# Optimization experiments

Hardware: AMD Instinct MI355X
Metric: run time of the kernel (lower is better)

Reference implementation:

```python
import jax, jax.numpy as jnp
import numpy as np

MARGIN = 0.3  # hard-coded in all three MarginRankingLoss instances


def setup_inputs() -> dict:
    key = jax.random.key(0)
    k1, k2, k3, k4 = jax.random.split(key, 4)
    n, d, num_ids = 4096, 2048, 100
    inputs = jax.random.normal(k1, (n, d), dtype=jnp.float32)
    targets_a = jax.random.randint(k2, (n,), 0, num_ids, dtype=jnp.int64)
    targets_b = jax.random.randint(k3, (n,), 0, num_ids, dtype=jnp.int64)
    lam = jax.random.uniform(k4, (), dtype=jnp.float32)
    epoch = 60
    return {"inputs": inputs, "targets_a": targets_a, "targets_b": targets_b,
            "lam": lam, "epoch": epoch}


def reference(inputs, targets_a, targets_b, lam, epoch):
    # pairwise euclidean distance: dist[i,j] = ||x_i - x_j||
    sq = jnp.sum(inputs * inputs, axis=1)                      # [n]
    dist = sq[:, None] + sq[None, :] - 2.0 * (inputs @ inputs.T)
    dist = jnp.sqrt(jnp.clip(dist, 1e-12))                     # [n, n]

    ma = targets_a[:, None] == targets_a[None, :]
    mb = targets_b[:, None] == targets_b[None, :]
    m_same_ab = ma & mb                                        # same a AND b (incl. diagonal)
    m_same_or = (ma & ~mb) | (~ma & mb)                        # exactly one of a/b matches
    m_dif_ab = ~ma & ~mb                                       # neither matches

    ninf = -jnp.inf
    pinf = jnp.inf
    hp = jnp.max(jnp.where(m_same_ab, dist, ninf), axis=1)     # hardest positive
    hn = jnp.min(jnp.where(m_dif_ab, dist, pinf), axis=1)      # hardest negative
    max_or = jnp.max(jnp.where(m_same_or, dist, ninf), axis=1)
    min_or = jnp.min(jnp.where(m_same_or, dist, pinf), axis=1)

    use_or = m_same_or.any(axis=1) & (epoch > 50)
    sp = jnp.where(use_or, max_or, hp)
    sn = jnp.where(use_or, min_or, hn)

    # MarginRankingLoss(x1, x2, y=1) = mean(relu(x2 - x1 + margin))
    loss_1 = jnp.mean(jnp.maximum(0.0, hp - hn + MARGIN))
    loss_2 = jnp.mean(jnp.maximum(0.0, sp - hn + MARGIN))
    loss_3 = jnp.mean(jnp.maximum(0.0, hp - sn + MARGIN))
    return loss_1 + loss_2 + loss_3
```

## Files before the change

### kernel.cpp

```cpp
#include <hip/hip_runtime.h>
#include <hip/hip_bf16.h>

#define NROW 4096
#define KDIM 2048
#define ROWB (KDIM * 2)
#define BT 256
#define BK 32
#define NT (KDIM / BK)
#define LDSBUF 32768
#define PHI(r) ((((r) >> 1) & 3) << 4)

typedef __attribute__((ext_vector_type(8))) short bf16x8;
typedef __attribute__((ext_vector_type(4))) float f32x4;
typedef __attribute__((ext_vector_type(4))) unsigned short u16x4;

__device__ __forceinline__ unsigned short f2bf(float x) {
    unsigned u = __float_as_uint(x);
    unsigned r = (u + 0x7FFFu + ((u >> 16) & 1u)) >> 16;
    return (unsigned short)r;
}
__device__ __forceinline__ float bf2f(unsigned short b) {
    return __uint_as_float(((unsigned)b) << 16);
}

__global__ __launch_bounds__(256) void k_convert(const float* __restrict__ X,
                                                 unsigned short* __restrict__ Xb,
                                                 float* __restrict__ sqv) {
    const int row = blockIdx.x;
    const int t = threadIdx.x;
    const float4* xr = (const float4*)(X + (size_t)row * KDIM);
    unsigned short* br = Xb + (size_t)row * KDIM;
    float acc = 0.f;
#pragma unroll
    for (int it = 0; it < 2; ++it) {
        int idx = t * 2 + it;
        float4 v = xr[idx];
        u16x4 b;
        b.x = f2bf(v.x); b.y = f2bf(v.y); b.z = f2bf(v.z); b.w = f2bf(v.w);
        float f0 = bf2f(b.x), f1 = bf2f(b.y), f2 = bf2f(b.z), f3 = bf2f(b.w);
        acc += f0 * f0 + f1 * f1 + f2 * f2 + f3 * f3;
        *(u16x4*)(br + idx * 4) = b;
    }
#pragma unroll
    for (int s = 32; s > 0; s >>= 1) acc += __shfl_xor(acc, s);
    __shared__ float red[4];
    const int lane = t & 63, wid = t >> 6;
    if (lane == 0) red[wid] = acc;
    __syncthreads();
    if (t == 0) sqv[row] = red[0] + red[1] + red[2] + red[3];
}

__global__ __launch_bounds__(256) void k_init(unsigned* hp, unsigned* hn,
                                              unsigned* mor, unsigned* mir,
                                              int* anyor, float* out) {
    int i = blockIdx.x * 256 + threadIdx.x;
    hp[i] = 0u;
    hn[i] = 0x7F800000u;
    mor[i] = 0u;
    mir[i] = 0x7F800000u;
    anyor[i] = 0;
    if (i == 0) out[0] = 0.f;
}

__global__ __launch_bounds__(512, 2) void k_gemm(const unsigned short* __restrict__ Xb,
                                                 const float* __restrict__ sqv,
                                                 const int* __restrict__ ta,
                                                 const int* __restrict__ tb,
                                                 unsigned int* __restrict__ hp,
                                                 unsigned int* __restrict__ hn,
                                                 unsigned int* __restrict__ mor,
                                                 unsigned int* __restrict__ mir,
                                                 int* __restrict__ anyor) {
    __shared__ char lds[3 * LDSBUF];
    const int bi = blockIdx.x >> 4;
    const int bj = blockIdx.x & 15;
    const int t = threadIdx.x;
    const int lane = t & 63;
    const int w = t >> 6;
    const int wm = w >> 2;
    const int wn = w & 3;
    const int l15 = lane & 15;
    const int k16 = (lane >> 4) * 16;

    const int srow = w * 16 + (lane >> 2);
    const int scol = (lane & 3) * 16;
    const char* xbase = (const char*)Xb;

    int aoffs[8], boffs[4];
#pragma unroll
    for (int m = 0; m < 8; ++m) {
        int r = wm * 128 + m * 16 + l15;
        aoffs[m] = r * 64 + (k16 ^ PHI(r));
    }
#pragma unroll
    for (int n = 0; n < 4; ++n) {
        int j = wn * 64 + n * 16 + l15;
        boffs[n] = 16384 + j * 64 + (k16 ^ PHI(j));
    }

    f32x4 acc[8][4] = {};

#define STAGE(tt, p)                                                          \
    do {                                                                      \
        const int isb_ = (p) >> 1, half_ = (p) & 1;                           \
        const int R_ = half_ * 128 + srow;                                    \
        const int gr_ = (isb_ ? bj : bi) * BT + R_;                           \
        const char* gsrc_ = xbase + (size_t)gr_ * ROWB + (size_t)(tt) * 64 +  \
                            (scol ^ PHI(R_));                                 \
        char* ldst_ = lds + ((tt) % 3) * LDSBUF + isb_ * 16384 + R_ * 64 + scol; \
        __builtin_amdgcn_global_load_lds(                                     \
            (const __attribute__((address_space(1))) void*)gsrc_,             \
            (__attribute__((address_space(3))) void*)ldst_, 16, 0, 0);        \
    } while (0)

#pragma unroll
    for (int p = 0; p < 4; ++p) STAGE(0, p);
#pragma unroll
    for (int p = 0; p < 4; ++p) STAGE(1, p);

    bf16x8 af[4], bfr[4];
    for (int tk = 0; tk < NT; ++tk) {
        if (tk < NT - 1)
            asm volatile("s_waitcnt vmcnt(4)" ::: "memory");
        else
            asm volatile("s_waitcnt vmcnt(0)" ::: "memory");
        __builtin_amdgcn_s_barrier();
        __builtin_amdgcn_sched_barrier(0);
        const char* Ab = lds + (tk % 3) * LDSBUF;
        const bool st = (tk + 2) < NT;
        const int t2 = tk + 2;

        if (st) STAGE(t2, 0);
#pragma unroll
        for (int m = 0; m < 4; ++m) af[m] = *(const bf16x8*)(Ab + aoffs[m]);
        bfr[0] = *(const bf16x8*)(Ab + boffs[0]);
        bfr[1] = *(const bf16x8*)(Ab + boffs[1]);
        __builtin_amdgcn_s_barrier();
        __builtin_amdgcn_s_setprio(1);
#pragma unroll
        for (int m = 0; m < 4; ++m) {
            acc[m][0] = __builtin_amdgcn_mfma_f32_16x16x32_bf16(af[m], bfr[0], acc[m][0], 0, 0, 0);
            acc[m][1] = __builtin_amdgcn_mfma_f32_16x16x32_bf16(af[m], bfr[1], acc[m][1], 0, 0, 0);
        }
        __builtin_amdgcn_s_setprio(0);
        __builtin_amdgcn_s_barrier();

        if (st) STAGE(t2, 1);
        bfr[2] = *(const bf16x8*)(Ab + boffs[2]);
        bfr[3] = *(const bf16x8*)(Ab + boffs[3]);
        __builtin_amdgcn_s_barrier();
        __builtin_amdgcn_s_setprio(1);
#pragma unroll
        for (int m = 0; m < 4; ++m) {
            acc[m][2] = __builtin_amdgcn_mfma_f32_16x16x32_bf16(af[m], bfr[2], acc[m][2], 0, 0, 0);
            acc[m][3] = __builtin_amdgcn_mfma_f32_16x16x32_bf16(af[m], bfr[3], acc[m][3], 0, 0, 0);
        }
        __builtin_amdgcn_s_setprio(0);
        __builtin_amdgcn_s_barrier();

        if (st) STAGE(t2, 2);
#pragma unroll
        for (int m = 0; m < 4; ++m) af[m] = *(const bf16x8*)(Ab + aoffs[4 + m]);
        __builtin_amdgcn_s_barrier();
        __builtin_amdgcn_s_setprio(1);
#pragma unroll
        for (int m = 0; m < 4; ++m) {
            acc[4 + m][2] = __builtin_amdgcn_mfma_f32_16x16x32_bf16(af[m], bfr[2], acc[4 + m][2], 0, 0, 0);
            acc[4 + m][3] = __builtin_amdgcn_mfma_f32_16x16x32_bf16(af[m], bfr[3], acc[4 + m][3], 0, 0, 0);
        }
        __builtin_amdgcn_s_setprio(0);
        __builtin_amdgcn_s_barrier();

        if (st) STAGE(t2, 3);
        __builtin_amdgcn_s_barrier();
        __builtin_amdgcn_s_setprio(1);
#pragma unroll
        for (int m = 0; m < 4; ++m) {
            acc[4 + m][0] = __builtin_amdgcn_mfma_f32_16x16x32_bf16(af[m], bfr[0], acc[4 + m][0], 0, 0, 0);
            acc[4 + m][1] = __builtin_amdgcn_mfma_f32_16x16x32_bf16(af[m], bfr[1], acc[4 + m][1], 0, 0, 0);
        }
        __builtin_amdgcn_s_setprio(0);
        __builtin_amdgcn_s_barrier();
    }
#undef STAGE

    float sqj[4];
    int taj[4], tbj[4];
#pragma unroll
    for (int n = 0; n < 4; ++n) {
        int j = bj * BT + wn * 64 + n * 16 + l15;
        sqj[n] = sqv[j];
        taj[n] = ta[j];
        tbj[n] = tb[j];
    }
    const float INF = __uint_as_float(0x7F800000u);
#pragma unroll
    for (int m = 0; m < 8; ++m) {
#pragma unroll
        for (int reg = 0; reg < 4; ++reg) {
            const int i = bi * BT + wm * 128 + m * 16 + (lane >> 4) * 4 + reg;
            const float sqi = sqv[i];
            const int tai = ta[i], tbi = tb[i];
            float vhp = 0.f, vhn = INF, vmor = 0.f, vmir = INF, vany = 0.f;
#pragma unroll
            for (int n = 0; n < 4; ++n) {
                float d2 = sqi + sqj[n] - 2.f * acc[m][n][reg];
                float d = sqrtf(fmaxf(d2, 1e-12f));
                bool ma = (tai == taj[n]), mb = (tbi == tbj[n]);
                if (ma && mb) {
                    vhp = fmaxf(vhp, d);
                } else if (ma != mb) {
                    vmor = fmaxf(vmor, d);
                    vmir = fminf(vmir, d);
                    vany = 1.f;
                } else {
                    vhn = fminf(vhn, d);
                }
            }
#pragma unroll
            for (int s = 1; s < 16; s <<= 1) {
                vhp = fmaxf(vhp, __shfl_xor(vhp, s, 16));
                vhn = fminf(vhn, __shfl_xor(vhn, s, 16));
                vmor = fmaxf(vmor, __shfl_xor(vmor, s, 16));
                vmir = fminf(vmir, __shfl_xor(vmir, s, 16));
                vany = fmaxf(vany, __shfl_xor(vany, s, 16));
            }
            if (l15 == 0) {
                if (vhp > 0.f) atomicMax(&hp[i], __float_as_uint(vhp));
                if (vhn < INF) atomicMin(&hn[i], __float_as_uint(vhn));
                if (vany > 0.f) {
                    atomicMax(&mor[i], __float_as_uint(vmor));
                    atomicMin(&mir[i], __float_as_uint(vmir));
                    atomicOr(&anyor[i], 1);
                }
            }
        }
    }
}

__global__ __launch_bounds__(256) void k_final(const unsigned* __restrict__ hp,
                                               const unsigned* __restrict__ hn,
                                               const unsigned* __restrict__ mor,
                                               const unsigned* __restrict__ mir,
                                               const int* __restrict__ anyor,
                                               const int* __restrict__ epoch_p,
                                               float* __restrict__ out) {
    const int t = threadIdx.x;
    const int i = blockIdx.x * 256 + t;
    const bool eok = (*epoch_p > 50);
    float fhp = __uint_as_float(hp[i]);
    float fhn = __uint_as_float(hn[i]);
    bool use_or = (anyor[i] != 0) && eok;
    float sp = use_or ? __uint_as_float(mor[i]) : fhp;
    float sn = use_or ? __uint_as_float(mir[i]) : fhn;
    float s = fmaxf(0.f, fhp - fhn + 0.3f) + fmaxf(0.f, sp - fhn + 0.3f) +
              fmaxf(0.f, fhp - sn + 0.3f);
#pragma unroll
    for (int sh = 32; sh > 0; sh >>= 1) s += __shfl_xor(s, sh);
    __shared__ float red[4];
    const int lane = t & 63, wid = t >> 6;
    if (lane == 0) red[wid] = s;
    __syncthreads();
    if (t == 0)
        atomicAdd(out, (red[0] + red[1] + red[2] + red[3]) * (1.f / 4096.f));
}

extern "C" void kernel_launch(void* const* d_in, const int* in_sizes, int n_in,
                              void* d_out, int out_size, void* d_ws, size_t ws_size,
                              hipStream_t stream) {
    const float* X = (const float*)d_in[0];
    const int* ta = (const int*)d_in[1];
    const int* tb = (const int*)d_in[2];
    const int* epoch_p = (const int*)d_in[4];
    float* out = (float*)d_out;

    char* ws = (char*)d_ws;
    unsigned short* Xb = (unsigned short*)ws;
    size_t off = (size_t)NROW * KDIM * sizeof(unsigned short);
    float* sqv = (float*)(ws + off); off += (size_t)NROW * 4;
    unsigned* hp = (unsigned*)(ws + off); off += (size_t)NROW * 4;
    unsigned* hn = (unsigned*)(ws + off); off += (size_t)NROW * 4;
    unsigned* mor = (unsigned*)(ws + off); off += (size_t)NROW * 4;
    unsigned* mir = (unsigned*)(ws + off); off += (size_t)NROW * 4;
    int* anyor = (int*)(ws + off); off += (size_t)NROW * 4;

    k_convert<<<NROW, 256, 0, stream>>>(X, Xb, sqv);
    k_init<<<NROW / 256, 256, 0, stream>>>(hp, hn, mor, mir, anyor, out);
    k_gemm<<<(NROW / BT) * (NROW / BT), 512, 0, stream>>>(Xb, sqv, ta, tb,
                                                          hp, hn, mor, mir, anyor);
    k_final<<<NROW / 256, 256, 0, stream>>>(hp, hn, mor, mir, anyor, epoch_p, out);
}
```

Before: 112.7 us.

## Double the K tile to 64 and switch GEMM to double-buffered LDS pipeline

The bf16 MFMA Gram-matrix kernel now loads K=64 per stage instead of 32. It uses two LDS buffers of 64 KB each instead of three of 32 KB, and the XOR swizzle is redone for 128-byte rows. Loads for the next tile are issued in two groups interleaved with the MFMA phases, using explicit vmcnt waits, which halves the number of loop iterations and barriers per K. This raises LDS use to 128 KB per block, which may limit the 2-blocks-per-CU launch bound, and it reduces prefetch depth from two tiles ahead to one.

```diff
diff --git a/kernel.cpp b/kernel.cpp
--- a/kernel.cpp
+++ b/kernel.cpp
@@ -5,10 +5,10 @@
 #define KDIM 2048
 #define ROWB (KDIM * 2)
 #define BT 256
-#define BK 32
+#define BK 64
 #define NT (KDIM / BK)
-#define LDSBUF 32768
-#define PHI(r) ((((r) >> 1) & 3) << 4)
+#define LDSBUF 65536
+#define PHI(r) (((r) & 7) << 4)
 
 typedef __attribute__((ext_vector_type(8))) short bf16x8;
 typedef __attribute__((ext_vector_type(4))) float f32x4;
@@ -71,7 +71,7 @@
                                                  unsigned int* __restrict__ mor,
                                                  unsigned int* __restrict__ mir,
                                                  int* __restrict__ anyor) {
-    __shared__ char lds[3 * LDSBUF];
+    __shared__ char lds[2 * LDSBUF];
     const int bi = blockIdx.x >> 4;
     const int bj = blockIdx.x & 15;
     const int t = threadIdx.x;
@@ -80,106 +80,124 @@
     const int wm = w >> 2;
     const int wn = w & 3;
     const int l15 = lane & 15;
-    const int k16 = (lane >> 4) * 16;
-
-    const int srow = w * 16 + (lane >> 2);
-    const int scol = (lane & 3) * 16;
+    const int kg16 = (lane >> 4) * 16;
     const char* xbase = (const char*)Xb;
 
-    int aoffs[8], boffs[4];
+    int aoff[8][2], boff[4][2];
 #pragma unroll
     for (int m = 0; m < 8; ++m) {
-        int r = wm * 128 + m * 16 + l15;
-        aoffs[m] = r * 64 + (k16 ^ PHI(r));
+        const int r = wm * 128 + m * 16 + l15;
+#pragma unroll
+        for (int ks = 0; ks < 2; ++ks)
+            aoff[m][ks] = r * 128 + ((ks * 64 + kg16) ^ PHI(r));
     }
 #pragma unroll
     for (int n = 0; n < 4; ++n) {
-        int j = wn * 64 + n * 16 + l15;
-        boffs[n] = 16384 + j * 64 + (k16 ^ PHI(j));
+        const int j = wn * 64 + n * 16 + l15;
+#pragma unroll
+        for (int ks = 0; ks < 2; ++ks)
+            boff[n][ks] = 32768 + j * 128 + ((ks * 64 + kg16) ^ PHI(j));
     }
 
     f32x4 acc[8][4] = {};
 
 #define STAGE(tt, p)                                                          \
     do {                                                                      \
-        const int isb_ = (p) >> 1, half_ = (p) & 1;                           \
-        const int R_ = half_ * 128 + srow;                                    \
-        const int gr_ = (isb_ ? bj : bi) * BT + R_;                           \
-        const char* gsrc_ = xbase + (size_t)gr_ * ROWB + (size_t)(tt) * 64 +  \
-                            (scol ^ PHI(R_));                                 \
-        char* ldst_ = lds + ((tt) % 3) * LDSBUF + isb_ * 16384 + R_ * 64 + scol; \
+        constexpr int isb_ = (p) >= 4;                                        \
+        constexpr int c_ = (p) - isb_ * 4;                                    \
+        const int row_ = c_ * 64 + (t >> 3);                                  \
+        const int gr_ = (isb_ ? bj : bi) * BT + row_;                         \
+        const char* gsrc_ = xbase + (size_t)gr_ * ROWB + (size_t)(tt) * 128 + \
+                            (((t & 7) * 16) ^ PHI(row_));                     \
+        char* ldst_ = lds + ((tt) & 1) * LDSBUF + isb_ * 32768 + row_ * 128 + \
+                      (t & 7) * 16;                                           \
         __builtin_amdgcn_global_load_lds(                                     \
             (const __attribute__((address_space(1))) void*)gsrc_,             \
             (__attribute__((address_space(3))) void*)ldst_, 16, 0, 0);        \
     } while (0)
 
-#pragma unroll
-    for (int p = 0; p < 4; ++p) STAGE(0, p);
-#pragma unroll
-    for (int p = 0; p < 4; ++p) STAGE(1, p);
-
-    bf16x8 af[4], bfr[4];
+    STAGE(0, 0); STAGE(0, 2); STAGE(0, 4); STAGE(0, 5);
+    STAGE(0, 6); STAGE(0, 7); STAGE(0, 1); STAGE(0, 3);
+    asm volatile("s_waitcnt vmcnt(2)" ::: "memory");
+    __builtin_amdgcn_s_barrier();
+
+    bf16x8 af[4][2], bfr[4][2];
     for (int tk = 0; tk < NT; ++tk) {
-        if (tk < NT - 1)
-            asm volatile("s_waitcnt vmcnt(4)" ::: "memory");
+        const char* bufb = lds + (tk & 1) * LDSBUF;
+        const bool stg = (tk + 1) < NT;
+
+        if (stg) { STAGE(tk + 1, 0); STAGE(tk + 1, 2); STAGE(tk + 1, 4); STAGE(tk + 1, 5); }
+#pragma unroll
+        for (int m = 0; m < 4; ++m) {
+            af[m][0] = *(const bf16x8*)(bufb + aoff[m][0]);
+            af[m][1] = *(const bf16x8*)(bufb + aoff[m][1]);
+        }
+#pragma unroll
+        for (int n = 0; n < 2; ++n) {
+            bfr[n][0] = *(const bf16x8*)(bufb + boff[n][0]);
+            bfr[n][1] = *(const bf16x8*)(bufb + boff[n][1]);
+        }
+        __builtin_amdgcn_s_barrier();
+        __builtin_amdgcn_s_setprio(1);
+#pragma unroll
+        for (int ks = 0; ks < 2; ++ks)
+#pragma unroll
+            for (int m = 0; m < 4; ++m) {
+                acc[m][0] = __builtin_amdgcn_mfma_f32_16x16x32_bf16(af[m][ks], bfr[0][ks], acc[m][0], 0, 0, 0);
+                acc[m][1] = __builtin_amdgcn_mfma_f32_16x16x32_bf16(af[m][ks], bfr[1][ks], acc[m][1], 0, 0, 0);
+            }
+        __builtin_amdgcn_s_setprio(0);
+        __builtin_amdgcn_s_barrier();
+
+        if (stg) { STAGE(tk + 1, 6); STAGE(tk + 1, 7); STAGE(tk + 1, 1); STAGE(tk + 1, 3); }
+#pragma unroll
+        for (int n = 2; n < 4; ++n) {
+            bfr[n][0] = *(const bf16x8*)(bufb + boff[n][0]);
+            bfr[n][1] = *(const bf16x8*)(bufb + boff[n][1]);
+        }
+        __builtin_amdgcn_s_barrier();
+        __builtin_amdgcn_s_setprio(1);
+#pragma unroll
+        for (int ks = 0; ks < 2; ++ks)
+#pragma unroll
+            for (int m = 0; m < 4; ++m) {
+                acc[m][2] = __builtin_amdgcn_mfma_f32_16x16x32_bf16(af[m][ks], bfr[2][ks], acc[m][2], 0, 0, 0);
+                acc[m][3] = __builtin_amdgcn_mfma_f32_16x16x32_bf16(af[m][ks], bfr[3][ks], acc[m][3], 0, 0, 0);
+            }
+        __builtin_amdgcn_s_setprio(0);
+        if (stg)
+            asm volatile("s_waitcnt vmcnt(8)" ::: "memory");
         else
             asm volatile("s_waitcnt vmcnt(0)" ::: "memory");
         __builtin_amdgcn_s_barrier();
-        __builtin_amdgcn_sched_barrier(0);
-        const char* Ab = lds + (tk % 3) * LDSBUF;
-        const bool st = (tk + 2) < NT;
-        const int t2 = tk + 2;
-
-        if (st) STAGE(t2, 0);
-#pragma unroll
-        for (int m = 0; m < 4; ++m) af[m] = *(const bf16x8*)(Ab + aoffs[m]);
-        bfr[0] = *(const bf16x8*)(Ab + boffs[0]);
-        bfr[1] = *(const bf16x8*)(Ab + boffs[1]);
+
+#pragma unroll
+        for (int m = 0; m < 4; ++m) {
+            af[m][0] = *(const bf16x8*)(bufb + aoff[4 + m][0]);
+            af[m][1] = *(const bf16x8*)(bufb + aoff[4 + m][1]);
+        }
         __builtin_amdgcn_s_barrier();
         __builtin_amdgcn_s_setprio(1);
 #pragma unroll
-        for (int m = 0; m < 4; ++m) {
-            acc[m][0] = __builtin_amdgcn_mfma_f32_16x16x32_bf16(af[m], bfr[0], acc[m][0], 0, 0, 0);
-            acc[m][1] = __builtin_amdgcn_mfma_f32_16x16x32_bf16(af[m], bfr[1], acc[m][1], 0, 0, 0);
-        }
+        for (int ks = 0; ks < 2; ++ks)
+#pragma unroll
+            for (int m = 0; m < 4; ++m) {
+                acc[4 + m][2] = __builtin_amdgcn_mfma_f32_16x16x32_bf16(af[m][ks], bfr[2][ks], acc[4 + m][2], 0, 0, 0);
+                acc[4 + m][3] = __builtin_amdgcn_mfma_f32_16x16x32_bf16(af[m][ks], bfr[3][ks], acc[4 + m][3], 0, 0, 0);
+            }
         __builtin_amdgcn_s_setprio(0);
         __builtin_amdgcn_s_barrier();
 
-        if (st) STAGE(t2, 1);
-        bfr[2] = *(const bf16x8*)(Ab + boffs[2]);
-        bfr[3] = *(const bf16x8*)(Ab + boffs[3]);
-        __builtin_amdgcn_s_barrier();
         __builtin_amdgcn_s_setprio(1);
 #pragma unroll
-        for (int m = 0; m < 4; ++m) {
-            acc[m][2] = __builtin_amdgcn_mfma_f32_16x16x32_bf16(af[m], bfr[2], acc[m][2], 0, 0, 0);
-            acc[m][3] = __builtin_amdgcn_mfma_f32_16x16x32_bf16(af[m], bfr[3], acc[m][3], 0, 0, 0);
-        }
+        for (int ks = 0; ks < 2; ++ks)
+#pragma unroll
+            for (int m = 0; m < 4; ++m) {
+                acc[4 + m][0] = __builtin_amdgcn_mfma_f32_16x16x32_bf16(af[m][ks], bfr[0][ks], acc[4 + m][0], 0, 0, 0);
+                acc[4 + m][1] = __builtin_amdgcn_mfma_f32_16x16x32_bf16(af[m][ks], bfr[1][ks], acc[4 + m][1], 0, 0, 0);
+            }
         __builtin_amdgcn_s_setprio(0);
-        __builtin_amdgcn_s_barrier();
-
-        if (st) STAGE(t2, 2);
-#pragma unroll
-        for (int m = 0; m < 4; ++m) af[m] = *(const bf16x8*)(Ab + aoffs[4 + m]);
-        __builtin_amdgcn_s_barrier();
-        __builtin_amdgcn_s_setprio(1);
-#pragma unroll
-        for (int m = 0; m < 4; ++m) {
-            acc[4 + m][2] = __builtin_amdgcn_mfma_f32_16x16x32_bf16(af[m], bfr[2], acc[4 + m][2], 0, 0, 0);
-            acc[4 + m][3] = __builtin_amdgcn_mfma_f32_16x16x32_bf16(af[m], bfr[3], acc[4 + m][3], 0, 0, 0);
-        }
-        __builtin_amdgcn_s_setprio(0);
-        __builtin_amdgcn_s_barrier();
-
-        if (st) STAGE(t2, 3);
-        __builtin_amdgcn_s_barrier();
-        __builtin_amdgcn_s_setprio(1);
-#pragma unroll
-        for (int m = 0; m < 4; ++m) {
-            acc[4 + m][0] = __builtin_amdgcn_mfma_f32_16x16x32_bf16(af[m], bfr[0], acc[4 + m][0], 0, 0, 0);
-            acc[4 + m][1] = __builtin_amdgcn_mfma_f32_16x16x32_bf16(af[m], bfr[1], acc[4 + m][1], 0, 0, 0);
-        }
-        __builtin_amdgcn_s_setprio(0);
+        if (stg) asm volatile("s_waitcnt vmcnt(2)" ::: "memory");
         __builtin_amdgcn_s_barrier();
     }
 #undef STAGE
```

Measured after the change: 109.6 us. -2.7%, faster.

## Simplify GEMM main loop and defer sqrt to final reduction on squared distances

Applied to the files above, without the earlier changes.

The interleaved four-phase main loop, with its many barriers and priority toggles, becomes a single phase per k-tile: all 8 A and 4 B fragments are read from LDS, the next tile is staged, then all 32 MFMAs issue, with rolling triple-buffer indices. The epilogue now reduces squared distances and applies sqrt only in k_final, since sqrt is monotonic, which removes 16M sqrt operations. The separate anyor flag is dropped and inferred from mor being nonzero, since a clamped distance is always positive. In exchange there are fewer barriers but more live fragment registers and less fine-grained overlap of LDS reads with MFMA.

```diff
diff --git a/kernel.cpp b/kernel.cpp
--- a/kernel.cpp
+++ b/kernel.cpp
@@ -7,12 +7,15 @@
 #define BT 256
 #define BK 32
 #define NT (KDIM / BK)
-#define LDSBUF 32768
+#define KTBUF 32768
+#define AB_OFF 16384
 #define PHI(r) ((((r) >> 1) & 3) << 4)
 
 typedef __attribute__((ext_vector_type(8))) short bf16x8;
 typedef __attribute__((ext_vector_type(4))) float f32x4;
 typedef __attribute__((ext_vector_type(4))) unsigned short u16x4;
+
+#define MFMA16(a, b, c) __builtin_amdgcn_mfma_f32_16x16x32_bf16((a), (b), (c), 0, 0, 0)
 
 __device__ __forceinline__ unsigned short f2bf(float x) {
     unsigned u = __float_as_uint(x);
@@ -52,13 +55,12 @@
 
 __global__ __launch_bounds__(256) void k_init(unsigned* hp, unsigned* hn,
                                               unsigned* mor, unsigned* mir,
-                                              int* anyor, float* out) {
+                                              float* out) {
     int i = blockIdx.x * 256 + threadIdx.x;
     hp[i] = 0u;
     hn[i] = 0x7F800000u;
     mor[i] = 0u;
     mir[i] = 0x7F800000u;
-    anyor[i] = 0;
     if (i == 0) out[0] = 0.f;
 }
 
@@ -69,9 +71,8 @@
                                                  unsigned int* __restrict__ hp,
                                                  unsigned int* __restrict__ hn,
                                                  unsigned int* __restrict__ mor,
-                                                 unsigned int* __restrict__ mir,
-                                                 int* __restrict__ anyor) {
-    __shared__ char lds[3 * LDSBUF];
+                                                 unsigned int* __restrict__ mir) {
+    __shared__ char lds[3 * KTBUF];
     const int bi = blockIdx.x >> 4;
     const int bj = blockIdx.x & 15;
     const int t = threadIdx.x;
@@ -80,107 +81,65 @@
     const int wm = w >> 2;
     const int wn = w & 3;
     const int l15 = lane & 15;
-    const int k16 = (lane >> 4) * 16;
-
-    const int srow = w * 16 + (lane >> 2);
-    const int scol = (lane & 3) * 16;
+    const int kg16 = (lane >> 4) * 16;
     const char* xbase = (const char*)Xb;
 
-    int aoffs[8], boffs[4];
-#pragma unroll
-    for (int m = 0; m < 8; ++m) {
-        int r = wm * 128 + m * 16 + l15;
-        aoffs[m] = r * 64 + (k16 ^ PHI(r));
-    }
-#pragma unroll
-    for (int n = 0; n < 4; ++n) {
-        int j = wn * 64 + n * 16 + l15;
-        boffs[n] = 16384 + j * 64 + (k16 ^ PHI(j));
-    }
+    const int swz = ((l15 >> 1) & 3) << 4;
+    const int akbase = (wm * 128 + l15) * 64 + (kg16 ^ swz);
+    const int bkbase = AB_OFF + (wn * 64 + l15) * 64 + (kg16 ^ swz);
 
     f32x4 acc[8][4] = {};
 
-#define STAGE(tt, p)                                                          \
+#define STAGE(tt, sb3)                                                        \
     do {                                                                      \
-        const int isb_ = (p) >> 1, half_ = (p) & 1;                           \
-        const int R_ = half_ * 128 + srow;                                    \
-        const int gr_ = (isb_ ? bj : bi) * BT + R_;                           \
-        const char* gsrc_ = xbase + (size_t)gr_ * ROWB + (size_t)(tt) * 64 +  \
-                            (scol ^ PHI(R_));                                 \
-        char* ldst_ = lds + ((tt) % 3) * LDSBUF + isb_ * 16384 + R_ * 64 + scol; \
-        __builtin_amdgcn_global_load_lds(                                     \
-            (const __attribute__((address_space(1))) void*)gsrc_,             \
-            (__attribute__((address_space(3))) void*)ldst_, 16, 0, 0);        \
+        _Pragma("unroll")                                                     \
+        for (int isb_ = 0; isb_ < 2; ++isb_) {                                \
+            _Pragma("unroll")                                                 \
+            for (int q_ = 0; q_ < 2; ++q_) {                                  \
+                const int row_ = q_ * 128 + (t >> 2);                         \
+                const int gr_ = (isb_ ? bj : bi) * BT + row_;                 \
+                const char* gsrc_ = xbase + (size_t)gr_ * ROWB +              \
+                                    (size_t)(tt) * 64 +                       \
+                                    (((t & 3) * 16) ^ PHI(row_));             \
+                char* ldst_ = lds + (sb3) * KTBUF + isb_ * AB_OFF +           \
+                              row_ * 64 + (t & 3) * 16;                       \
+                __builtin_amdgcn_global_load_lds(                             \
+                    (const __attribute__((address_space(1))) void*)gsrc_,     \
+                    (__attribute__((address_space(3))) void*)ldst_, 16, 0, 0);\
+            }                                                                 \
+        }                                                                     \
     } while (0)
 
-#pragma unroll
-    for (int p = 0; p < 4; ++p) STAGE(0, p);
-#pragma unroll
-    for (int p = 0; p < 4; ++p) STAGE(1, p);
-
-    bf16x8 af[4], bfr[4];
+    STAGE(0, 0);
+    STAGE(1, 1);
+
+    int r3 = 0, s3 = 2;
     for (int tk = 0; tk < NT; ++tk) {
         if (tk < NT - 1)
             asm volatile("s_waitcnt vmcnt(4)" ::: "memory");
         else
             asm volatile("s_waitcnt vmcnt(0)" ::: "memory");
         __builtin_amdgcn_s_barrier();
-        __builtin_amdgcn_sched_barrier(0);
-        const char* Ab = lds + (tk % 3) * LDSBUF;
-        const bool st = (tk + 2) < NT;
-        const int t2 = tk + 2;
-
-        if (st) STAGE(t2, 0);
-#pragma unroll
-        for (int m = 0; m < 4; ++m) af[m] = *(const bf16x8*)(Ab + aoffs[m]);
-        bfr[0] = *(const bf16x8*)(Ab + boffs[0]);
-        bfr[1] = *(const bf16x8*)(Ab + boffs[1]);
-        __builtin_amdgcn_s_barrier();
-        __builtin_amdgcn_s_setprio(1);
-#pragma unroll
-        for (int m = 0; m < 4; ++m) {
-            acc[m][0] = __builtin_amdgcn_mfma_f32_16x16x32_bf16(af[m], bfr[0], acc[m][0], 0, 0, 0);
-            acc[m][1] = __builtin_amdgcn_mfma_f32_16x16x32_bf16(af[m], bfr[1], acc[m][1], 0, 0, 0);
-        }
-        __builtin_amdgcn_s_setprio(0);
-        __builtin_amdgcn_s_barrier();
-
-        if (st) STAGE(t2, 1);
-        bfr[2] = *(const bf16x8*)(Ab + boffs[2]);
-        bfr[3] = *(const bf16x8*)(Ab + boffs[3]);
-        __builtin_amdgcn_s_barrier();
-        __builtin_amdgcn_s_setprio(1);
-#pragma unroll
-        for (int m = 0; m < 4; ++m) {
-            acc[m][2] = __builtin_amdgcn_mfma_f32_16x16x32_bf16(af[m], bfr[2], acc[m][2], 0, 0, 0);
-            acc[m][3] = __builtin_amdgcn_mfma_f32_16x16x32_bf16(af[m], bfr[3], acc[m][3], 0, 0, 0);
-        }
-        __builtin_amdgcn_s_setprio(0);
-        __builtin_amdgcn_s_barrier();
-
-        if (st) STAGE(t2, 2);
-#pragma unroll
-        for (int m = 0; m < 4; ++m) af[m] = *(const bf16x8*)(Ab + aoffs[4 + m]);
-        __builtin_amdgcn_s_barrier();
-        __builtin_amdgcn_s_setprio(1);
-#pragma unroll
-        for (int m = 0; m < 4; ++m) {
-            acc[4 + m][2] = __builtin_amdgcn_mfma_f32_16x16x32_bf16(af[m], bfr[2], acc[4 + m][2], 0, 0, 0);
-            acc[4 + m][3] = __builtin_amdgcn_mfma_f32_16x16x32_bf16(af[m], bfr[3], acc[4 + m][3], 0, 0, 0);
-        }
-        __builtin_amdgcn_s_setprio(0);
-        __builtin_amdgcn_s_barrier();
-
-        if (st) STAGE(t2, 3);
-        __builtin_amdgcn_s_barrier();
-        __builtin_amdgcn_s_setprio(1);
-#pragma unroll
-        for (int m = 0; m < 4; ++m) {
-            acc[4 + m][0] = __builtin_amdgcn_mfma_f32_16x16x32_bf16(af[m], bfr[0], acc[4 + m][0], 0, 0, 0);
-            acc[4 + m][1] = __builtin_amdgcn_mfma_f32_16x16x32_bf16(af[m], bfr[1], acc[4 + m][1], 0, 0, 0);
-        }
-        __builtin_amdgcn_s_setprio(0);
-        __builtin_amdgcn_s_barrier();
+
+        const char* buf = lds + r3 * KTBUF;
+        bf16x8 af[8], bfr[4];
+#pragma unroll
+        for (int m = 0; m < 8; ++m)
+            af[m] = *(const bf16x8*)(buf + akbase + m * 1024);
+#pragma unroll
+        for (int n = 0; n < 4; ++n)
+            bfr[n] = *(const bf16x8*)(buf + bkbase + n * 1024);
+
+        if (tk + 2 < NT) STAGE(tk + 2, s3);
+
+#pragma unroll
+        for (int m = 0; m < 8; ++m)
+#pragma unroll
+            for (int n = 0; n < 4; ++n)
+                acc[m][n] = MFMA16(af[m], bfr[n], acc[m][n]);
+
+        r3 = (r3 == 2) ? 0 : r3 + 1;
+        s3 = (s3 == 2) ? 0 : s3 + 1;
     }
 #undef STAGE
 
@@ -201,37 +160,33 @@
             const int i = bi * BT + wm * 128 + m * 16 + (lane >> 4) * 4 + reg;
             const float sqi = sqv[i];
             const int tai = ta[i], tbi = tb[i];
-            float vhp = 0.f, vhn = INF, vmor = 0.f, vmir = INF, vany = 0.f;
+            float vhp = 0.f, vhn = INF, vmo = 0.f, vmi = INF;
 #pragma unroll
             for (int n = 0; n < 4; ++n) {
-                float d2 = sqi + sqj[n] - 2.f * acc[m][n][reg];
-                float d = sqrtf(fmaxf(d2, 1e-12f));
+                float d2 = fmaxf(sqi + sqj[n] - 2.f * acc[m][n][reg], 1e-12f);
                 bool ma = (tai == taj[n]), mb = (tbi == tbj[n]);
                 if (ma && mb) {
-                    vhp = fmaxf(vhp, d);
+                    vhp = fmaxf(vhp, d2);
                 } else if (ma != mb) {
-                    vmor = fmaxf(vmor, d);
-                    vmir = fminf(vmir, d);
-                    vany = 1.f;
+                    vmo = fmaxf(vmo, d2);
+                    vmi = fminf(vmi, d2);
                 } else {
-                    vhn = fminf(vhn, d);
+                    vhn = fminf(vhn, d2);
                 }
             }
 #pragma unroll
             for (int s = 1; s < 16; s <<= 1) {
                 vhp = fmaxf(vhp, __shfl_xor(vhp, s, 16));
                 vhn = fminf(vhn, __shfl_xor(vhn, s, 16));
-                vmor = fmaxf(vmor, __shfl_xor(vmor, s, 16));
-                vmir = fminf(vmir, __shfl_xor(vmir, s, 16));
-                vany = fmaxf(vany, __shfl_xor(vany, s, 16));
+                vmo = fmaxf(vmo, __shfl_xor(vmo, s, 16));
+                vmi = fminf(vmi, __shfl_xor(vmi, s, 16));
             }
             if (l15 == 0) {
                 if (vhp > 0.f) atomicMax(&hp[i], __float_as_uint(vhp));
                 if (vhn < INF) atomicMin(&hn[i], __float_as_uint(vhn));
-                if (vany > 0.f) {
-                    atomicMax(&mor[i], __float_as_uint(vmor));
-                    atomicMin(&mir[i], __float_as_uint(vmir));
-                    atomicOr(&anyor[i], 1);
+                if (vmo > 0.f) {
+                    atomicMax(&mor[i], __float_as_uint(vmo));
+                    atomicMin(&mir[i], __float_as_uint(vmi));
                 }
             }
         }
@@ -242,17 +197,17 @@
                                                const unsigned* __restrict__ hn,
                                                const unsigned* __restrict__ mor,
                                                const unsigned* __restrict__ mir,
-                                               const int* __restrict__ anyor,
                                                const int* __restrict__ epoch_p,
                                                float* __restrict__ out) {
     const int t = threadIdx.x;
     const int i = blockIdx.x * 256 + t;
     const bool eok = (*epoch_p > 50);
-    float fhp = __uint_as_float(hp[i]);
-    float fhn = __uint_as_float(hn[i]);
-    bool use_or = (anyor[i] != 0) && eok;
-    float sp = use_or ? __uint_as_float(mor[i]) : fhp;
-    float sn = use_or ? __uint_as_float(mir[i]) : fhn;
+    const unsigned morb = mor[i];
+    float fhp = sqrtf(__uint_as_float(hp[i]));
+    float fhn = sqrtf(__uint_as_float(hn[i]));
+    bool use_or = (morb != 0u) && eok;
+    float sp = use_or ? sqrtf(__uint_as_float(morb)) : fhp;
+    float sn = use_or ? sqrtf(__uint_as_float(mir[i])) : fhn;
     float s = fmaxf(0.f, fhp - fhn + 0.3f) + fmaxf(0.f, sp - fhn + 0.3f) +
               fmaxf(0.f, fhp - sn + 0.3f);
 #pragma unroll
@@ -282,11 +237,10 @@
     unsigned* hn = (unsigned*)(ws + off); off += (size_t)NROW * 4;
     unsigned* mor = (unsigned*)(ws + off); off += (size_t)NROW * 4;
     unsigned* mir = (unsigned*)(ws + off); off += (size_t)NROW * 4;
-    int* anyor = (int*)(ws + off); off += (size_t)NROW * 4;
 
     k_convert<<<NROW, 256, 0, stream>>>(X, Xb, sqv);
-    k_init<<<NROW / 256, 256, 0, stream>>>(hp, hn, mor, mir, anyor, out);
+    k_init<<<NROW / 256, 256, 0, stream>>>(hp, hn, mor, mir, out);
     k_gemm<<<(NROW / BT) * (NROW / BT), 512, 0, stream>>>(Xb, sqv, ta, tb,
-                                                          hp, hn, mor, mir, anyor);
-    k_final<<<NROW / 256, 256, 0, stream>>>(hp, hn, mor, mir, anyor, epoch_p, out);
-}
+                                                          hp, hn, mor, mir);
+    k_final<<<NROW / 256, 256, 0, stream>>>(hp, hn, mor, mir, epoch_p, out);
+}
```

Result: faster. 100.3 us (-11.0%).
